# Kernel optimization log

Hardware: AMD Instinct MI355X
Metric: run time of the kernel (lower is better)

The kernel has to match this reference:

```python
import jax, jax.numpy as jnp
import numpy as np

N = 100000   # nodes
E = 400000   # edges (before self-loops)
G = 4000     # graphs in batch
F_IN = 32    # node_embedding
HID = 128    # hidden_channels
H = 3        # heads (hard-coded in module)
W3 = H * HID # 384, post-concat width
NC = 10      # num_classes
NL = 4       # num_layers
NEG_SLOPE = 0.2


def _lin(key, fan_in, fan_out):
    return jax.random.normal(key, (fan_in, fan_out), jnp.float32) * (1.0 / np.sqrt(fan_in))


def setup_inputs() -> dict:
    key = jax.random.key(0)
    ks = iter(jax.random.split(key, 40))
    x = jax.random.normal(next(ks), (N, F_IN), jnp.float32)
    edge_index = jax.random.randint(next(ks), (2, E), 0, N, dtype=jnp.int32)
    batch = jnp.sort(jax.random.randint(next(ks), (N,), 0, G, dtype=jnp.int32))
    inp = dict(x=x, edge_index=edge_index, batch=batch)
    # MLP stem
    inp['lin1_w'] = _lin(next(ks), F_IN, 2 * HID); inp['lin1_b'] = jnp.zeros((2 * HID,), jnp.float32)
    inp['lin2_w'] = _lin(next(ks), 2 * HID, HID);  inp['lin2_b'] = jnp.zeros((HID,), jnp.float32)
    # conv1: GATConv(HID -> HID, heads=3)
    inp['w0'] = _lin(next(ks), HID, W3)
    inp['as0'] = jax.random.normal(next(ks), (H, HID), jnp.float32) * 0.1
    inp['ad0'] = jax.random.normal(next(ks), (H, HID), jnp.float32) * 0.1
    inp['b0'] = jnp.zeros((W3,), jnp.float32)
    # remaining NL-1 convs: GATConv(W3 -> HID, heads=3), stacked
    inp['wl'] = jnp.stack([_lin(next(ks), W3, W3) for _ in range(NL - 1)])
    inp['asl'] = jax.random.normal(next(ks), (NL - 1, H, HID), jnp.float32) * 0.1
    inp['adl'] = jax.random.normal(next(ks), (NL - 1, H, HID), jnp.float32) * 0.1
    inp['bl'] = jnp.zeros((NL - 1, W3), jnp.float32)
    # batch norms (NL total, all width W3)
    inp['gamma'] = jnp.ones((NL, W3), jnp.float32)
    inp['beta'] = jnp.zeros((NL, W3), jnp.float32)
    # head
    inp['lin3_w'] = _lin(next(ks), W3, HID); inp['lin3_b'] = jnp.zeros((HID,), jnp.float32)
    inp['lin4_w'] = _lin(next(ks), HID, NC); inp['lin4_b'] = jnp.zeros((NC,), jnp.float32)
    return inp


def _gat(x, W, a_src, a_dst, bias, src, dst):
    # PyG GATConv, concat heads. x: [N, Fin]
    h = (x @ W).reshape(N, H, HID)                       # [N, H, C]
    es = jnp.einsum('nhc,hc->nh', h, a_src)              # [N, H]
    ed = jnp.einsum('nhc,hc->nh', h, a_dst)
    e = jax.nn.leaky_relu(es[src] + ed[dst], NEG_SLOPE)  # [Etot, H]
    m = jax.ops.segment_max(e, dst, num_segments=N)      # segment softmax over incoming edges
    p = jnp.exp(e - m[dst])
    s = jax.ops.segment_sum(p, dst, num_segments=N)
    alpha = p / s[dst]                                   # every node has a self-loop -> s>0
    out = jax.ops.segment_sum(alpha[:, :, None] * h[src], dst, num_segments=N)
    return out.reshape(N, W3) + bias


def _bn(x, g, b):
    mu = x.mean(0)
    var = x.var(0)
    return (x - mu) * jax.lax.rsqrt(var + 1e-5) * g + b


def reference(x, edge_index, batch, lin1_w, lin1_b, lin2_w, lin2_b,
              w0, as0, ad0, b0, wl, asl, adl, bl, gamma, beta,
              lin3_w, lin3_b, lin4_w, lin4_b):
    loop = jnp.arange(N, dtype=edge_index.dtype)
    src = jnp.concatenate([edge_index[0], loop])  # add_self_loops=True (PyG default)
    dst = jnp.concatenate([edge_index[1], loop])
    h = jax.nn.relu(x @ lin1_w + lin1_b)
    h = jax.nn.relu(h @ lin2_w + lin2_b)
    h = _gat(h, w0, as0, ad0, b0, src, dst)
    h = _bn(h, gamma[0], beta[0])
    for i in range(NL - 1):
        h = _gat(h, wl[i], asl[i], adl[i], bl[i], src, dst)
        h = _bn(h, gamma[i + 1], beta[i + 1])
    # global mean pool over graphs
    sums = jax.ops.segment_sum(h, batch, num_segments=G)
    cnt = jax.ops.segment_sum(jnp.ones((N,), h.dtype), batch, num_segments=G)
    g = sums / jnp.maximum(cnt, 1.0)[:, None]
    g = jax.nn.relu(g @ lin3_w + lin3_b)
    logits = g @ lin4_w + lin4_b
    return jax.nn.log_softmax(logits, axis=-1)
```

## Files before the change

### kernel.cpp

```cpp
#include <hip/hip_runtime.h>

#define NN      100000
#define NN2     100096
#define NE      400000
#define ETOT    500000
#define NG      4000
#define W3D     384
#define HIDD    128
#define NCLS    10
#define NSLICE  256

typedef unsigned short u16;
typedef unsigned int   u32;
typedef unsigned long long u64;
typedef __attribute__((ext_vector_type(8))) short short8;
typedef __attribute__((ext_vector_type(4))) float f32x4;

static __device__ __forceinline__ float bf2f(u16 u) {
  return __uint_as_float(((u32)u) << 16);
}
static __device__ __forceinline__ float bflo(u32 u) {
  return __uint_as_float(u << 16);
}
static __device__ __forceinline__ float bfhi(u32 u) {
  return __uint_as_float(u & 0xffff0000u);
}
static __device__ __forceinline__ u16 f2b(float f) {
  u32 u = __float_as_uint(f);
  u32 r = (u + 0x7fffu + ((u >> 16) & 1u)) >> 16;
  return (u16)r;
}

static __device__ __forceinline__ void llds16(const u16* g, u16* l) {
  __builtin_amdgcn_global_load_lds(
      (const __attribute__((address_space(1))) void*)(u64)(const void*)g,
      (__attribute__((address_space(3))) void*)(u64)(void*)l, 16, 0, 0);
}

__global__ void mg_zero_out(float* out, int n) {
  int i = blockIdx.x * 256 + threadIdx.x;
  if (i < n) out[i] = 0.f;
}

__global__ void mg_cvt_x(const float* __restrict__ x, u16* __restrict__ Xb) {
  int idx = blockIdx.x * 256 + threadIdx.x;
  if (idx >= NN2 * 64) return;
  int row = idx >> 6, col = idx & 63;
  Xb[idx] = (row < NN && col < 32) ? f2b(x[row * 32 + col]) : (u16)0;
}

__global__ void mg_transpose_pad(const float* __restrict__ in, u16* __restrict__ out,
                                 int K, int Nn, int Kpad) {
  int idx = blockIdx.x * 256 + threadIdx.x;
  if (idx >= Nn * Kpad) return;
  int n = idx / Kpad, k = idx - n * Kpad;
  out[idx] = (k < K) ? f2b(in[k * Nn + n]) : (u16)0;
}

__global__ void mg_fold_w(const u16* __restrict__ Wt, const float* __restrict__ scale,
                          const float* __restrict__ shift, u16* __restrict__ Wp,
                          float* __restrict__ bp) {
  __shared__ float red[128];
  int j = blockIdx.x, t = threadIdx.x;
  const u16* src = Wt + (size_t)j * W3D;
  u16* dst = Wp + (size_t)j * W3D;
  float acc = 0.f;
  for (int k = t; k < W3D; k += 128) {
    float w = bf2f(src[k]);
    dst[k] = f2b(w * scale[k]);
    acc += w * shift[k];
  }
  red[t] = acc; __syncthreads();
  for (int off = 64; off; off >>= 1) {
    if (t < off) red[t] += red[t + off];
    __syncthreads();
  }
  if (t == 0) bp[j] = red[0];
}

__global__ void mg_edge_histo(const int* __restrict__ ei, int* __restrict__ deg) {
  int e = blockIdx.x * 256 + threadIdx.x;
  if (e >= ETOT) return;
  int d = (e < NE) ? ei[NE + e] : (e - NE);
  atomicAdd(&deg[d], 1);
}

__global__ void mg_scan1(const int* __restrict__ in, int* __restrict__ bsum, int n) {
  __shared__ int sd[256];
  int tid = threadIdx.x;
  int base = blockIdx.x * 1024 + tid * 4;
  int s = 0;
#pragma unroll
  for (int j = 0; j < 4; ++j) { int i = base + j; if (i < n) s += in[i]; }
  sd[tid] = s; __syncthreads();
  for (int off = 128; off > 0; off >>= 1) {
    if (tid < off) sd[tid] += sd[tid + off];
    __syncthreads();
  }
  if (tid == 0) bsum[blockIdx.x] = sd[0];
}

__global__ void mg_scan2(int* __restrict__ bsum, int nb) {
  __shared__ int sd[256];
  int tid = threadIdx.x;
  int v = (tid < nb) ? bsum[tid] : 0;
  sd[tid] = v; __syncthreads();
  for (int off = 1; off < 256; off <<= 1) {
    int t = (tid >= off) ? sd[tid - off] : 0;
    __syncthreads();
    sd[tid] += t;
    __syncthreads();
  }
  if (tid < nb) bsum[tid] = sd[tid] - v;
}

__global__ void mg_scan3(const int* __restrict__ in, const int* __restrict__ bexcl,
                         int* __restrict__ out, int n) {
  __shared__ int sd[256];
  int tid = threadIdx.x;
  int base = blockIdx.x * 1024 + tid * 4;
  int loc[4]; int s = 0;
#pragma unroll
  for (int j = 0; j < 4; ++j) { int i = base + j; loc[j] = (i < n) ? in[i] : 0; s += loc[j]; }
  sd[tid] = s; __syncthreads();
  for (int off = 1; off < 256; off <<= 1) {
    int t = (tid >= off) ? sd[tid - off] : 0;
    __syncthreads();
    sd[tid] += t;
    __syncthreads();
  }
  int run = sd[tid] - s + bexcl[blockIdx.x];
#pragma unroll
  for (int j = 0; j < 4; ++j) {
    int i = base + j;
    if (i < n) { out[i] = run; run += loc[j]; if (i == n - 1) out[n] = run; }
  }
}

__global__ void mg_edge_scatter(const int* __restrict__ ei, int* __restrict__ fill,
                                int* __restrict__ colsrc) {
  int e = blockIdx.x * 256 + threadIdx.x;
  if (e >= ETOT) return;
  int s, d;
  if (e < NE) { s = ei[e]; d = ei[NE + e]; } else { s = e - NE; d = s; }
  int pos = atomicAdd(&fill[d], 1);
  colsrc[pos] = s;
}

__global__ void mg_graph_ptr(const int* __restrict__ batch, int* __restrict__ gptr) {
  int g = blockIdx.x * 256 + threadIdx.x;
  if (g > NG) return;
  if (g == NG) { gptr[NG] = NN; return; }
  int lo = 0, hi = NN;
  while (lo < hi) { int mid = (lo + hi) >> 1; if (batch[mid] < g) lo = mid + 1; else hi = mid; }
  gptr[g] = lo;
}

#define GBM 128
#define GBN 128
#define GBK 32
#define CP  130

__global__ __launch_bounds__(256) void mg_gemm(
    const u16* __restrict__ Ag, const u16* __restrict__ Bt,
    int Mstore, int Nn, int K,
    u16* __restrict__ Cb, const float* __restrict__ bias, int relu,
    const float* __restrict__ asrc, const float* __restrict__ adst,
    float* __restrict__ aes, float* __restrict__ aed) {
  __shared__ u16 lds[17408];
  int tid = threadIdx.x;
  int n0 = blockIdx.x * GBN, m0 = blockIdx.y * GBM;
  int lane = tid & 63, wv = tid >> 6;
  int mw = (wv & 1) * 64, nw = (wv >> 1) * 64;
  int lr = lane & 15, lq = lane >> 4;
  int rr = lane & 15, cc4 = lane >> 4;

  f32x4 acc[4][4];
#pragma unroll
  for (int mi = 0; mi < 4; ++mi)
#pragma unroll
    for (int ni = 0; ni < 4; ++ni) acc[mi][ni] = (f32x4){0.f, 0.f, 0.f, 0.f};

  const u16* aB = Ag + (size_t)m0 * K + cc4 * 8;
  const u16* bB = Bt + (size_t)n0 * K + cc4 * 8;
  int niter = K >> 5;

#pragma unroll
  for (int j = 0; j < 2; ++j) {
    int sg = wv * 2 + j, grow = sg * 16 + rr;
    llds16(aB + (size_t)grow * K, lds + sg * 512);
    llds16(bB + (size_t)grow * K, lds + 8192 + sg * 512);
  }

  for (int it = 0; it < niter; ++it) {
    __syncthreads();
    if (it + 1 < niter) {
      int k0 = (it + 1) * GBK, b = (it + 1) & 1;
#pragma unroll
      for (int j = 0; j < 2; ++j) {
        int sg = wv * 2 + j, grow = sg * 16 + rr;
        llds16(aB + (size_t)grow * K + k0, lds + b * 4096 + sg * 512);
        llds16(bB + (size_t)grow * K + k0, lds + 8192 + b * 4096 + sg * 512);
      }
    }
    const u16* Al = lds + (it & 1) * 4096;
    const u16* Bl = lds + 8192 + (it & 1) * 4096;
    short8 af[4], bfr[4];
#pragma unroll
    for (int mi = 0; mi < 4; ++mi)
      af[mi] = *(const short8*)(Al + ((mw >> 4) + mi) * 512 + lq * 128 + lr * 8);
#pragma unroll
    for (int ni = 0; ni < 4; ++ni)
      bfr[ni] = *(const short8*)(Bl + ((nw >> 4) + ni) * 512 + lq * 128 + lr * 8);
#pragma unroll
    for (int mi = 0; mi < 4; ++mi)
#pragma unroll
      for (int ni = 0; ni < 4; ++ni)
        acc[mi][ni] = __builtin_amdgcn_mfma_f32_16x16x32_bf16(af[mi], bfr[ni], acc[mi][ni], 0, 0, 0);
  }
  __syncthreads();

  float bvv[4];
#pragma unroll
  for (int ni = 0; ni < 4; ++ni)
    bvv[ni] = bias ? bias[n0 + nw + ni * 16 + lr] : 0.f;

#pragma unroll
  for (int mi = 0; mi < 4; ++mi)
#pragma unroll
    for (int ni = 0; ni < 4; ++ni) {
      int cl = nw + ni * 16 + lr;
      int rb = mw + mi * 16 + lq * 4;
#pragma unroll
      for (int r = 0; r < 4; ++r) {
        float v = acc[mi][ni][r] + bvv[ni];
        if (relu) v = fmaxf(v, 0.f);
        lds[(rb + r) * CP + cl] = f2b(v);
      }
    }
  __syncthreads();

  int rowl = tid >> 1, half = (tid & 1) * 64;
  const u16* src = lds + rowl * CP + half;
  uint4 creg[8];
#pragma unroll
  for (int j = 0; j < 8; ++j) creg[j] = *(const uint4*)(src + j * 8);
  u16* gout = Cb + (size_t)(m0 + rowl) * Nn + n0 + half;
#pragma unroll
  for (int j = 0; j < 8; ++j) *(uint4*)(gout + j * 8) = creg[j];

  if (aes) {
    const float* ap = asrc + n0 + half;
    const float* dp = adst + n0 + half;
    float se = 0.f, de = 0.f;
#pragma unroll
    for (int j = 0; j < 8; ++j) {
      float4 a0 = *(const float4*)(ap + j * 8);
      float4 a1 = *(const float4*)(ap + j * 8 + 4);
      float4 d0 = *(const float4*)(dp + j * 8);
      float4 d1 = *(const float4*)(dp + j * 8 + 4);
      uint4 rv = creg[j];
      float v0 = bflo(rv.x), v1 = bfhi(rv.x), v2 = bflo(rv.y), v3 = bfhi(rv.y);
      float v4 = bflo(rv.z), v5 = bfhi(rv.z), v6 = bflo(rv.w), v7 = bfhi(rv.w);
      se += v0 * a0.x + v1 * a0.y + v2 * a0.z + v3 * a0.w
          + v4 * a1.x + v5 * a1.y + v6 * a1.z + v7 * a1.w;
      de += v0 * d0.x + v1 * d0.y + v2 * d0.z + v3 * d0.w
          + v4 * d1.x + v5 * d1.y + v6 * d1.z + v7 * d1.w;
    }
    se += __shfl_xor(se, 1);
    de += __shfl_xor(de, 1);
    int row = m0 + rowl;
    if ((tid & 1) == 0 && row < Mstore) {
      aes[row * 4 + blockIdx.x] = se;
      aed[row * 4 + blockIdx.x] = de;
    }
  }
}

__global__ __launch_bounds__(256) void mg_aggregate(
    const u16* __restrict__ B, const float* __restrict__ es,
    const float* __restrict__ ed, const int* __restrict__ rowptr,
    const int* __restrict__ colsrc, const float* __restrict__ bias,
    u16* __restrict__ A, float* __restrict__ stats) {
  __shared__ float bS[4 * W3D];
  __shared__ float bQ[4 * W3D];
  int wv = threadIdx.x >> 6, lane = threadIdx.x & 63;
  if (lane < 48) {
    int h = lane >> 4;
    int cc = lane * 8;
    float4 bv0 = *(const float4*)(bias + cc);
    float4 bv1 = *(const float4*)(bias + cc + 4);
    float stS[8], stQ[8];
#pragma unroll
    for (int j = 0; j < 8; ++j) { stS[j] = 0.f; stQ[j] = 0.f; }
#pragma unroll
    for (int sub = 0; sub < 2; ++sub) {
      int n = blockIdx.x * 8 + wv * 2 + sub;
      int r0 = rowptr[n], r1 = rowptr[n + 1];
      float4 edv = *(const float4*)(ed + 4 * n);
      float4 esn = *(const float4*)(es + 4 * n);
      float s0 = esn.x + edv.x; s0 = (s0 > 0.f) ? s0 : 0.2f * s0;
      float s1 = esn.y + edv.y; s1 = (s1 > 0.f) ? s1 : 0.2f * s1;
      float s2 = esn.z + edv.z; s2 = (s2 > 0.f) ? s2 : 0.2f * s2;
      float mh  = (h == 0) ? s0 : ((h == 1) ? s1 : s2);
      float edh = (h == 0) ? edv.x : ((h == 1) ? edv.y : edv.z);
      float accv[8];
#pragma unroll
      for (int j = 0; j < 8; ++j) accv[j] = 0.f;
      float ssum = 0.f;
      int sA = __builtin_amdgcn_readfirstlane(colsrc[r0]);
      float4 evA = *(const float4*)(es + 4 * sA);
      uint4  rvA = *(const uint4*)(B + (size_t)sA * W3D + cc);
      float4 evB = evA; uint4 rvB = rvA;
      if (r0 + 1 < r1) {
        int sB = __builtin_amdgcn_readfirstlane(colsrc[r0 + 1]);
        evB = *(const float4*)(es + 4 * sB);
        rvB = *(const uint4*)(B + (size_t)sB * W3D + cc);
      }
      for (int r = r0; r < r1; ++r) {
        float4 ev = evA; uint4 rv = rvA;
        evA = evB; rvA = rvB;
        if (r + 2 < r1) {
          int sC = __builtin_amdgcn_readfirstlane(colsrc[r + 2]);
          evB = *(const float4*)(es + 4 * sC);
          rvB = *(const uint4*)(B + (size_t)sC * W3D + cc);
        }
        float e = ((h == 0) ? ev.x : ((h == 1) ? ev.y : ev.z)) + edh;
        e = (e > 0.f) ? e : 0.2f * e;
        float p = __expf(e - mh);
        ssum += p;
        accv[0] += p * bflo(rv.x); accv[1] += p * bfhi(rv.x);
        accv[2] += p * bflo(rv.y); accv[3] += p * bfhi(rv.y);
        accv[4] += p * bflo(rv.z); accv[5] += p * bfhi(rv.z);
        accv[6] += p * bflo(rv.w); accv[7] += p * bfhi(rv.w);
      }
      float inv = 1.0f / ssum;
      float v[8];
      v[0] = accv[0] * inv + bv0.x; v[1] = accv[1] * inv + bv0.y;
      v[2] = accv[2] * inv + bv0.z; v[3] = accv[3] * inv + bv0.w;
      v[4] = accv[4] * inv + bv1.x; v[5] = accv[5] * inv + bv1.y;
      v[6] = accv[6] * inv + bv1.z; v[7] = accv[7] * inv + bv1.w;
      uint4 st;
      st.x = (u32)f2b(v[0]) | ((u32)f2b(v[1]) << 16);
      st.y = (u32)f2b(v[2]) | ((u32)f2b(v[3]) << 16);
      st.z = (u32)f2b(v[4]) | ((u32)f2b(v[5]) << 16);
      st.w = (u32)f2b(v[6]) | ((u32)f2b(v[7]) << 16);
      *(uint4*)(A + (size_t)n * W3D + cc) = st;
#pragma unroll
      for (int j = 0; j < 8; ++j) { stS[j] += v[j]; stQ[j] += v[j] * v[j]; }
    }
    *(float4*)(bS + wv * W3D + cc)     = (float4){stS[0], stS[1], stS[2], stS[3]};
    *(float4*)(bS + wv * W3D + cc + 4) = (float4){stS[4], stS[5], stS[6], stS[7]};
    *(float4*)(bQ + wv * W3D + cc)     = (float4){stQ[0], stQ[1], stQ[2], stQ[3]};
    *(float4*)(bQ + wv * W3D + cc + 4) = (float4){stQ[4], stQ[5], stQ[6], stQ[7]};
  }
  __syncthreads();
  for (int t = threadIdx.x; t < W3D; t += 256) {
    float s = 0.f, q = 0.f;
#pragma unroll
    for (int w = 0; w < 4; ++w) { s += bS[w * W3D + t]; q += bQ[w * W3D + t]; }
    float* sl = stats + (size_t)(blockIdx.x & (NSLICE - 1)) * 768;
    atomicAdd(&sl[t], s);
    atomicAdd(&sl[W3D + t], q);
  }
}

__global__ void mg_bn_finalize(const float* __restrict__ stats, const float* __restrict__ gamma,
                               const float* __restrict__ beta, float* __restrict__ scale,
                               float* __restrict__ shift) {
  int c = threadIdx.x;
  float s = 0.f, q = 0.f;
  for (int b = 0; b < NSLICE; ++b) { s += stats[b * 768 + c]; q += stats[b * 768 + W3D + c]; }
  const float invN = 1.0f / (float)NN;
  float mu = s * invN;
  float var = fmaxf(q * invN - mu * mu, 0.f);
  float inv = rsqrtf(var + 1e-5f);
  float g = gamma[c], be = beta[c];
  scale[c] = g * inv;
  shift[c] = be - mu * g * inv;
}

__global__ void mg_pool(const u16* __restrict__ A, const float* __restrict__ scale,
                        const float* __restrict__ shift, const int* __restrict__ gptr,
                        float* __restrict__ pooled) {
  int g = blockIdx.x, c = threadIdx.x;
  int r0 = gptr[g], r1 = gptr[g + 1];
  float acc = 0.f;
  for (int n = r0; n < r1; ++n) acc += bf2f(A[(size_t)n * W3D + c]);
  int cnt = r1 - r0;
  float v = (cnt > 0) ? (acc / (float)cnt) * scale[c] + shift[c] : 0.f;
  pooled[g * W3D + c] = v;
}

__global__ void mg_head(const float* __restrict__ pooled, const float* __restrict__ w3,
                        const float* __restrict__ b3, const float* __restrict__ w4,
                        const float* __restrict__ b4, float* __restrict__ out) {
  __shared__ float p[W3D];
  __shared__ float g2[HIDD];
  __shared__ float lg[NCLS];
  int g = blockIdx.x, t = threadIdx.x;
  for (int i = t; i < W3D; i += 128) p[i] = pooled[g * W3D + i];
  __syncthreads();
  float acc = 0.f;
  for (int k = 0; k < W3D; ++k) acc += p[k] * w3[k * HIDD + t];
  g2[t] = fmaxf(acc + b3[t], 0.f);
  __syncthreads();
  if (t < NCLS) {
    float a = 0.f;
    for (int k = 0; k < HIDD; ++k) a += g2[k] * w4[k * NCLS + t];
    lg[t] = a + b4[t];
  }
  __syncthreads();
  if (t < NCLS) {
    float m = -1e30f;
#pragma unroll
    for (int j = 0; j < NCLS; ++j) m = fmaxf(m, lg[j]);
    float se = 0.f;
#pragma unroll
    for (int j = 0; j < NCLS; ++j) se += __expf(lg[j] - m);
    out[g * NCLS + t] = lg[t] - m - __logf(se);
  }
}

extern "C" void kernel_launch(void* const* d_in, const int* in_sizes, int n_in,
                              void* d_out, int out_size, void* d_ws, size_t ws_size,
                              hipStream_t stream) {
  const float* x     = (const float*)d_in[0];
  const int*   ei    = (const int*)d_in[1];
  const int*   batch = (const int*)d_in[2];
  const float* w1    = (const float*)d_in[3];
  const float* b1    = (const float*)d_in[4];
  const float* w2    = (const float*)d_in[5];
  const float* b2    = (const float*)d_in[6];
  const float* w0    = (const float*)d_in[7];
  const float* as0   = (const float*)d_in[8];
  const float* ad0   = (const float*)d_in[9];
  const float* b0    = (const float*)d_in[10];
  const float* wl    = (const float*)d_in[11];
  const float* asl   = (const float*)d_in[12];
  const float* adl   = (const float*)d_in[13];
  const float* bl    = (const float*)d_in[14];
  const float* gamma = (const float*)d_in[15];
  const float* beta  = (const float*)d_in[16];
  const float* w3    = (const float*)d_in[17];
  const float* b3    = (const float*)d_in[18];
  const float* w4    = (const float*)d_in[19];
  const float* b4    = (const float*)d_in[20];
  float* out = (float*)d_out;

  char* w = (char*)d_ws;
  auto alloc = [&](size_t bytes) -> void* {
    void* p = (void*)w;
    w += (bytes + 255) & ~(size_t)255;
    return p;
  };
  u16*   P      = (u16*)alloc((size_t)NN2 * W3D * 2);
  u16*   Q      = (u16*)alloc((size_t)NN2 * W3D * 2);
  float* es     = (float*)alloc((size_t)NN * 4 * 4);
  float* ed     = (float*)alloc((size_t)NN * 4 * 4);
  int*   deg    = (int*)alloc((size_t)NN * 4);
  int*   rowptr = (int*)alloc((size_t)(NN + 1) * 4);
  int*   fill   = (int*)alloc((size_t)NN * 4);
  int*   colsrc = (int*)alloc((size_t)ETOT * 4);
  int*   bsum   = (int*)alloc(256 * 4);
  float* stats  = (float*)alloc((size_t)NSLICE * 768 * 4);
  float* scale  = (float*)alloc(W3D * 4);
  float* shift  = (float*)alloc(W3D * 4);
  float* bprime = (float*)alloc(W3D * 4);
  int*   gptr   = (int*)alloc((size_t)(NG + 1) * 4);
  float* pooled = (float*)alloc((size_t)NG * W3D * 4);
  u16*   W1T    = (u16*)alloc(256 * 64 * 2);
  u16*   W2T    = (u16*)alloc(128 * 256 * 2);
  u16*   W0T    = (u16*)alloc(384 * 128 * 2);
  u16*   WlT    = (u16*)alloc((size_t)3 * 384 * 384 * 2);
  u16*   WpT    = (u16*)alloc((size_t)384 * 384 * 2);
  u16*   Xb     = Q;

  if ((size_t)(w - (char*)d_ws) > ws_size) {
    mg_zero_out<<<(out_size + 255) / 256, 256, 0, stream>>>(out, out_size);
    return;
  }

  mg_cvt_x<<<(NN2 * 64 + 255) / 256, 256, 0, stream>>>(x, Xb);
  mg_transpose_pad<<<(256 * 64 + 255) / 256, 256, 0, stream>>>(w1, W1T, 32, 256, 64);
  mg_transpose_pad<<<(128 * 256 + 255) / 256, 256, 0, stream>>>(w2, W2T, 256, 128, 256);
  mg_transpose_pad<<<(384 * 128 + 255) / 256, 256, 0, stream>>>(w0, W0T, 128, 384, 128);
  for (int i = 0; i < 3; ++i)
    mg_transpose_pad<<<(384 * 384 + 255) / 256, 256, 0, stream>>>(
        wl + (size_t)i * 384 * 384, WlT + (size_t)i * 384 * 384, 384, 384, 384);

  hipMemsetAsync(deg, 0, (size_t)NN * 4, stream);
  mg_edge_histo<<<(ETOT + 255) / 256, 256, 0, stream>>>(ei, deg);
  int nb = (NN + 1023) / 1024;
  mg_scan1<<<nb, 256, 0, stream>>>(deg, bsum, NN);
  mg_scan2<<<1, 256, 0, stream>>>(bsum, nb);
  mg_scan3<<<nb, 256, 0, stream>>>(deg, bsum, rowptr, NN);
  hipMemcpyAsync(fill, rowptr, (size_t)NN * 4, hipMemcpyDeviceToDevice, stream);
  mg_edge_scatter<<<(ETOT + 255) / 256, 256, 0, stream>>>(ei, fill, colsrc);
  mg_graph_ptr<<<(NG + 1 + 255) / 256, 256, 0, stream>>>(batch, gptr);

  dim3 blk(256);
  int mtiles = NN2 / GBM;

  mg_gemm<<<dim3(2, mtiles), blk, 0, stream>>>(Xb, W1T, NN, 256, 64,
                                               P, b1, 1,
                                               nullptr, nullptr, nullptr, nullptr);
  mg_gemm<<<dim3(1, mtiles), blk, 0, stream>>>(P, W2T, NN, 128, 256,
                                               Q, b2, 1,
                                               nullptr, nullptr, nullptr, nullptr);

  for (int i = 0; i < 4; ++i) {
    int K = (i == 0) ? 128 : 384;
    const u16* Bt;
    const float* bi_g = nullptr;
    if (i == 0) {
      Bt = W0T;
    } else {
      mg_fold_w<<<384, 128, 0, stream>>>(WlT + (size_t)(i - 1) * 384 * 384,
                                         scale, shift, WpT, bprime);
      Bt = WpT;
      bi_g = bprime;
    }
    const float* as = (i == 0) ? as0 : (asl + (size_t)(i - 1) * 384);
    const float* ad = (i == 0) ? ad0 : (adl + (size_t)(i - 1) * 384);
    const float* bi = (i == 0) ? b0  : (bl  + (size_t)(i - 1) * 384);
    hipMemsetAsync(stats, 0, (size_t)NSLICE * 768 * 4, stream);
    mg_gemm<<<dim3(3, mtiles), blk, 0, stream>>>(Q, Bt, NN, W3D, K,
                                                 P, bi_g, 0,
                                                 as, ad, es, ed);
    mg_aggregate<<<NN / 8, blk, 0, stream>>>(P, es, ed, rowptr, colsrc, bi, Q, stats);
    mg_bn_finalize<<<1, 384, 0, stream>>>(stats, gamma + (size_t)i * W3D,
                                          beta + (size_t)i * W3D, scale, shift);
  }

  mg_pool<<<NG, 384, 0, stream>>>(Q, scale, shift, gptr, pooled);
  mg_head<<<NG, 128, 0, stream>>>(pooled, w3, b3, w4, b4, out);
}
```

Measured before the change: 1.118 ms.

## Use 8-wave GEMM blocks and interleave two nodes' edge loops in aggregation

Result: slower. 1.292 ms (+15.5%).

```diff
diff --git a/kernel.cpp b/kernel.cpp
--- a/kernel.cpp
+++ b/kernel.cpp
@@ -161,7 +161,7 @@
 #define GBK 32
 #define CP  130
 
-__global__ __launch_bounds__(256) void mg_gemm(
+__global__ __launch_bounds__(512, 6) void mg_gemm(
     const u16* __restrict__ Ag, const u16* __restrict__ Bt,
     int Mstore, int Nn, int K,
     u16* __restrict__ Cb, const float* __restrict__ bias, int relu,
@@ -171,64 +171,57 @@
   int tid = threadIdx.x;
   int n0 = blockIdx.x * GBN, m0 = blockIdx.y * GBM;
   int lane = tid & 63, wv = tid >> 6;
-  int mw = (wv & 1) * 64, nw = (wv >> 1) * 64;
+  int mw = (wv & 1) * 64, nw = (wv >> 1) * 32;
   int lr = lane & 15, lq = lane >> 4;
   int rr = lane & 15, cc4 = lane >> 4;
 
-  f32x4 acc[4][4];
+  f32x4 acc[4][2];
 #pragma unroll
   for (int mi = 0; mi < 4; ++mi)
 #pragma unroll
-    for (int ni = 0; ni < 4; ++ni) acc[mi][ni] = (f32x4){0.f, 0.f, 0.f, 0.f};
+    for (int ni = 0; ni < 2; ++ni) acc[mi][ni] = (f32x4){0.f, 0.f, 0.f, 0.f};
 
   const u16* aB = Ag + (size_t)m0 * K + cc4 * 8;
   const u16* bB = Bt + (size_t)n0 * K + cc4 * 8;
   int niter = K >> 5;
-
-#pragma unroll
-  for (int j = 0; j < 2; ++j) {
-    int sg = wv * 2 + j, grow = sg * 16 + rr;
-    llds16(aB + (size_t)grow * K, lds + sg * 512);
-    llds16(bB + (size_t)grow * K, lds + 8192 + sg * 512);
-  }
+  int grow = wv * 16 + rr;
+
+  llds16(aB + (size_t)grow * K, lds + wv * 512);
+  llds16(bB + (size_t)grow * K, lds + 8192 + wv * 512);
 
   for (int it = 0; it < niter; ++it) {
     __syncthreads();
     if (it + 1 < niter) {
       int k0 = (it + 1) * GBK, b = (it + 1) & 1;
-#pragma unroll
-      for (int j = 0; j < 2; ++j) {
-        int sg = wv * 2 + j, grow = sg * 16 + rr;
-        llds16(aB + (size_t)grow * K + k0, lds + b * 4096 + sg * 512);
-        llds16(bB + (size_t)grow * K + k0, lds + 8192 + b * 4096 + sg * 512);
-      }
+      llds16(aB + (size_t)grow * K + k0, lds + b * 4096 + wv * 512);
+      llds16(bB + (size_t)grow * K + k0, lds + 8192 + b * 4096 + wv * 512);
     }
     const u16* Al = lds + (it & 1) * 4096;
     const u16* Bl = lds + 8192 + (it & 1) * 4096;
-    short8 af[4], bfr[4];
+    short8 af[4], bfr[2];
 #pragma unroll
     for (int mi = 0; mi < 4; ++mi)
       af[mi] = *(const short8*)(Al + ((mw >> 4) + mi) * 512 + lq * 128 + lr * 8);
 #pragma unroll
-    for (int ni = 0; ni < 4; ++ni)
+    for (int ni = 0; ni < 2; ++ni)
       bfr[ni] = *(const short8*)(Bl + ((nw >> 4) + ni) * 512 + lq * 128 + lr * 8);
 #pragma unroll
     for (int mi = 0; mi < 4; ++mi)
 #pragma unroll
-      for (int ni = 0; ni < 4; ++ni)
+      for (int ni = 0; ni < 2; ++ni)
         acc[mi][ni] = __builtin_amdgcn_mfma_f32_16x16x32_bf16(af[mi], bfr[ni], acc[mi][ni], 0, 0, 0);
   }
   __syncthreads();
 
-  float bvv[4];
-#pragma unroll
-  for (int ni = 0; ni < 4; ++ni)
+  float bvv[2];
+#pragma unroll
+  for (int ni = 0; ni < 2; ++ni)
     bvv[ni] = bias ? bias[n0 + nw + ni * 16 + lr] : 0.f;
 
 #pragma unroll
   for (int mi = 0; mi < 4; ++mi)
 #pragma unroll
-    for (int ni = 0; ni < 4; ++ni) {
+    for (int ni = 0; ni < 2; ++ni) {
       int cl = nw + ni * 16 + lr;
       int rb = mw + mi * 16 + lq * 4;
 #pragma unroll
@@ -240,21 +233,21 @@
     }
   __syncthreads();
 
-  int rowl = tid >> 1, half = (tid & 1) * 64;
-  const u16* src = lds + rowl * CP + half;
-  uint4 creg[8];
-#pragma unroll
-  for (int j = 0; j < 8; ++j) creg[j] = *(const uint4*)(src + j * 8);
-  u16* gout = Cb + (size_t)(m0 + rowl) * Nn + n0 + half;
-#pragma unroll
-  for (int j = 0; j < 8; ++j) *(uint4*)(gout + j * 8) = creg[j];
+  int rowl = tid >> 2, q = (tid & 3) * 32;
+  const u16* src = lds + rowl * CP + q;
+  uint4 creg[4];
+#pragma unroll
+  for (int j = 0; j < 4; ++j) creg[j] = *(const uint4*)(src + j * 8);
+  u16* gout = Cb + (size_t)(m0 + rowl) * Nn + n0 + q;
+#pragma unroll
+  for (int j = 0; j < 4; ++j) *(uint4*)(gout + j * 8) = creg[j];
 
   if (aes) {
-    const float* ap = asrc + n0 + half;
-    const float* dp = adst + n0 + half;
+    const float* ap = asrc + n0 + q;
+    const float* dp = adst + n0 + q;
     float se = 0.f, de = 0.f;
 #pragma unroll
-    for (int j = 0; j < 8; ++j) {
+    for (int j = 0; j < 4; ++j) {
       float4 a0 = *(const float4*)(ap + j * 8);
       float4 a1 = *(const float4*)(ap + j * 8 + 4);
       float4 d0 = *(const float4*)(dp + j * 8);
@@ -267,10 +260,10 @@
       de += v0 * d0.x + v1 * d0.y + v2 * d0.z + v3 * d0.w
           + v4 * d1.x + v5 * d1.y + v6 * d1.z + v7 * d1.w;
     }
-    se += __shfl_xor(se, 1);
-    de += __shfl_xor(de, 1);
+    se += __shfl_xor(se, 1); se += __shfl_xor(se, 2);
+    de += __shfl_xor(de, 1); de += __shfl_xor(de, 2);
     int row = m0 + rowl;
-    if ((tid & 1) == 0 && row < Mstore) {
+    if ((tid & 3) == 0 && row < Mstore) {
       aes[row * 4 + blockIdx.x] = se;
       aed[row * 4 + blockIdx.x] = de;
     }
@@ -293,53 +286,70 @@
     float stS[8], stQ[8];
 #pragma unroll
     for (int j = 0; j < 8; ++j) { stS[j] = 0.f; stQ[j] = 0.f; }
-#pragma unroll
-    for (int sub = 0; sub < 2; ++sub) {
-      int n = blockIdx.x * 8 + wv * 2 + sub;
-      int r0 = rowptr[n], r1 = rowptr[n + 1];
+
+    int   rA[2], cnt[2];
+    float mh[2], edh[2], ssum[2];
+    float accv[2][8];
+    float4 evP[2][2]; uint4 rvP[2][2];
+#pragma unroll
+    for (int s = 0; s < 2; ++s) {
+      int n = blockIdx.x * 8 + wv * 2 + s;
+      rA[s] = rowptr[n];
+      cnt[s] = rowptr[n + 1] - rA[s];
       float4 edv = *(const float4*)(ed + 4 * n);
       float4 esn = *(const float4*)(es + 4 * n);
       float s0 = esn.x + edv.x; s0 = (s0 > 0.f) ? s0 : 0.2f * s0;
       float s1 = esn.y + edv.y; s1 = (s1 > 0.f) ? s1 : 0.2f * s1;
       float s2 = esn.z + edv.z; s2 = (s2 > 0.f) ? s2 : 0.2f * s2;
-      float mh  = (h == 0) ? s0 : ((h == 1) ? s1 : s2);
-      float edh = (h == 0) ? edv.x : ((h == 1) ? edv.y : edv.z);
-      float accv[8];
-#pragma unroll
-      for (int j = 0; j < 8; ++j) accv[j] = 0.f;
-      float ssum = 0.f;
-      int sA = __builtin_amdgcn_readfirstlane(colsrc[r0]);
-      float4 evA = *(const float4*)(es + 4 * sA);
-      uint4  rvA = *(const uint4*)(B + (size_t)sA * W3D + cc);
-      float4 evB = evA; uint4 rvB = rvA;
-      if (r0 + 1 < r1) {
-        int sB = __builtin_amdgcn_readfirstlane(colsrc[r0 + 1]);
-        evB = *(const float4*)(es + 4 * sB);
-        rvB = *(const uint4*)(B + (size_t)sB * W3D + cc);
+      mh[s]  = (h == 0) ? s0 : ((h == 1) ? s1 : s2);
+      edh[s] = (h == 0) ? edv.x : ((h == 1) ? edv.y : edv.z);
+      ssum[s] = 0.f;
+#pragma unroll
+      for (int j = 0; j < 8; ++j) accv[s][j] = 0.f;
+      int sA = __builtin_amdgcn_readfirstlane(colsrc[rA[s]]);
+      evP[s][0] = *(const float4*)(es + 4 * sA);
+      rvP[s][0] = *(const uint4*)(B + (size_t)sA * W3D + cc);
+      evP[s][1] = evP[s][0]; rvP[s][1] = rvP[s][0];
+      if (cnt[s] > 1) {
+        int sB = __builtin_amdgcn_readfirstlane(colsrc[rA[s] + 1]);
+        evP[s][1] = *(const float4*)(es + 4 * sB);
+        rvP[s][1] = *(const uint4*)(B + (size_t)sB * W3D + cc);
       }
-      for (int r = r0; r < r1; ++r) {
-        float4 ev = evA; uint4 rv = rvA;
-        evA = evB; rvA = rvB;
-        if (r + 2 < r1) {
-          int sC = __builtin_amdgcn_readfirstlane(colsrc[r + 2]);
-          evB = *(const float4*)(es + 4 * sC);
-          rvB = *(const uint4*)(B + (size_t)sC * W3D + cc);
+    }
+
+    while (cnt[0] > 0 || cnt[1] > 0) {
+#pragma unroll
+      for (int s = 0; s < 2; ++s) {
+        if (cnt[s] > 0) {
+          float4 ev = evP[s][0]; uint4 rv = rvP[s][0];
+          evP[s][0] = evP[s][1]; rvP[s][0] = rvP[s][1];
+          if (cnt[s] > 2) {
+            int nx = __builtin_amdgcn_readfirstlane(colsrc[rA[s] + 2]);
+            evP[s][1] = *(const float4*)(es + 4 * nx);
+            rvP[s][1] = *(const uint4*)(B + (size_t)nx * W3D + cc);
+          }
+          ++rA[s]; --cnt[s];
+          float e = ((h == 0) ? ev.x : ((h == 1) ? ev.y : ev.z)) + edh[s];
+          e = (e > 0.f) ? e : 0.2f * e;
+          float p = __expf(e - mh[s]);
+          ssum[s] += p;
+          accv[s][0] += p * bflo(rv.x); accv[s][1] += p * bfhi(rv.x);
+          accv[s][2] += p * bflo(rv.y); accv[s][3] += p * bfhi(rv.y);
+          accv[s][4] += p * bflo(rv.z); accv[s][5] += p * bfhi(rv.z);
+          accv[s][6] += p * bflo(rv.w); accv[s][7] += p * bfhi(rv.w);
         }
-        float e = ((h == 0) ? ev.x : ((h == 1) ? ev.y : ev.z)) + edh;
-        e = (e > 0.f) ? e : 0.2f * e;
-        float p = __expf(e - mh);
-        ssum += p;
-        accv[0] += p * bflo(rv.x); accv[1] += p * bfhi(rv.x);
-        accv[2] += p * bflo(rv.y); accv[3] += p * bfhi(rv.y);
-        accv[4] += p * bflo(rv.z); accv[5] += p * bfhi(rv.z);
-        accv[6] += p * bflo(rv.w); accv[7] += p * bfhi(rv.w);
       }
-      float inv = 1.0f / ssum;
+    }
+
+#pragma unroll
+    for (int s = 0; s < 2; ++s) {
+      int n = blockIdx.x * 8 + wv * 2 + s;
+      float inv = 1.0f / ssum[s];
       float v[8];
-      v[0] = accv[0] * inv + bv0.x; v[1] = accv[1] * inv + bv0.y;
-      v[2] = accv[2] * inv + bv0.z; v[3] = accv[3] * inv + bv0.w;
-      v[4] = accv[4] * inv + bv1.x; v[5] = accv[5] * inv + bv1.y;
-      v[6] = accv[6] * inv + bv1.z; v[7] = accv[7] * inv + bv1.w;
+      v[0] = accv[s][0] * inv + bv0.x; v[1] = accv[s][1] * inv + bv0.y;
+      v[2] = accv[s][2] * inv + bv0.z; v[3] = accv[s][3] * inv + bv0.w;
+      v[4] = accv[s][4] * inv + bv1.x; v[5] = accv[s][5] * inv + bv1.y;
+      v[6] = accv[s][6] * inv + bv1.z; v[7] = accv[s][7] * inv + bv1.w;
       uint4 st;
       st.x = (u32)f2b(v[0]) | ((u32)f2b(v[1]) << 16);
       st.y = (u32)f2b(v[2]) | ((u32)f2b(v[3]) << 16);
@@ -499,7 +509,7 @@
   mg_edge_scatter<<<(ETOT + 255) / 256, 256, 0, stream>>>(ei, fill, colsrc);
   mg_graph_ptr<<<(NG + 1 + 255) / 256, 256, 0, stream>>>(batch, gptr);
 
-  dim3 blk(256);
+  dim3 blk(512);
   int mtiles = NN2 / GBM;
 
   mg_gemm<<<dim3(2, mtiles), blk, 0, stream>>>(Xb, W1T, NN, 256, 64,
@@ -528,7 +538,7 @@
     mg_gemm<<<dim3(3, mtiles), blk, 0, stream>>>(Q, Bt, NN, W3D, K,
                                                  P, bi_g, 0,
                                                  as, ad, es, ed);
-    mg_aggregate<<<NN / 8, blk, 0, stream>>>(P, es, ed, rowptr, colsrc, bi, Q, stats);
+    mg_aggregate<<<NN / 8, 256, 0, stream>>>(P, es, ed, rowptr, colsrc, bi, Q, stats);
     mg_bn_finalize<<<1, 384, 0, stream>>>(stats, gamma + (size_t)i * W3D,
                                           beta + (size_t)i * W3D, scale, shift);
   }
```
